# Kernel optimization log

Hardware: AMD Instinct MI355X
Metric: run time of the kernel (lower is better)

Reference implementation:

```python
import jax, jax.numpy as jnp
import numpy as np

B, T, E, H = 4, 2048, 1024, 16
HS = E // H  # head_size = 64


def setup_inputs() -> dict:
    key = jax.random.key(0)
    ks = jax.random.split(key, 5)
    x = jax.random.normal(ks[0], (B, T, E), jnp.float32)
    scale = 0.02
    Wq = jax.random.normal(ks[1], (H, E, HS), jnp.float32) * scale
    Wk = jax.random.normal(ks[2], (H, E, HS), jnp.float32) * scale
    Wv = jax.random.normal(ks[3], (H, E, HS), jnp.float32) * scale
    Wo = jax.random.normal(ks[4], (E, E), jnp.float32) * scale
    bo = jnp.zeros((E,), jnp.float32)
    return {"x": x, "Wq": Wq, "Wk": Wk, "Wv": Wv, "Wo": Wo, "bo": bo}


def reference(x, Wq, Wk, Wv, Wo, bo):
    b, t, e = x.shape
    # per-head projections, batched over heads
    Q = jnp.einsum('bte,hed->bhtd', x, Wq)  # (B,H,T,HS)
    K = jnp.einsum('bte,hed->bhtd', x, Wk)
    V = jnp.einsum('bte,hed->bhtd', x, Wv)
    # faithful quirk 1: scale by sqrt(embd_size), not sqrt(head_size)
    scores = jnp.einsum('bhtd,bhsd->bhts', Q, K) / jnp.sqrt(jnp.float32(e))
    mask = jnp.tril(jnp.ones((t, t), dtype=bool))  # (T_q, T_k)
    scores = jnp.where(mask[None, None, :, :], scores, -jnp.inf)
    # faithful quirk 2: original softmaxes over dim=1 of (B,Tq,Tk) = the QUERY axis
    attn = jax.nn.softmax(scores, axis=2)
    out = jnp.einsum('bhts,bhsd->bhtd', attn, V)  # (B,H,T,HS)
    out = out.transpose(0, 2, 1, 3).reshape(b, t, e)  # concat heads -> (B,T,E)
    return out @ Wo + bo
```

## Files before the change

kernel.cpp:

```cpp
#include <hip/hip_runtime.h>
#include <stdint.h>

#define Bn 4
#define Tn 2048
#define En 1024
#define Hn 16
#define HSn 64
#define BHn (Bn*Hn)
#define NRn (Bn*Tn)

#define CEXP 0.0450840831f

typedef __attribute__((ext_vector_type(8))) short short8;
typedef __attribute__((ext_vector_type(4))) float f32x4;
typedef __attribute__((ext_vector_type(16))) float f32x16;
typedef __attribute__((ext_vector_type(4))) unsigned int uint4w;

__device__ __forceinline__ unsigned short f2b(float f){
  union { float f; unsigned int u; } c; c.f = f;
  unsigned int u = c.u + 0x7FFFu + ((c.u >> 16) & 1u);
  return (unsigned short)(u >> 16);
}
__device__ __forceinline__ float b2f(unsigned short s){
  union { unsigned int u; float f; } c; c.u = ((unsigned int)s) << 16;
  return c.f;
}
__device__ __forceinline__ unsigned int cvtpk(float lo, float hi){
  unsigned int r;
  asm("v_cvt_pk_bf16_f32 %0, %1, %2" : "=v"(r) : "v"(lo), "v"(hi));
  return r;
}
__device__ __forceinline__ f32x4 mfma16(short8 a, short8 b, f32x4 c){
  return __builtin_amdgcn_mfma_f32_16x16x32_bf16(a, b, c, 0, 0, 0);
}
__device__ __forceinline__ f32x16 mfma32(short8 a, short8 b, f32x16 c){
  return __builtin_amdgcn_mfma_f32_32x32x16_bf16(a, b, c, 0, 0, 0);
}
__device__ __forceinline__ void gl16(const void* g, void* s){
  __builtin_amdgcn_global_load_lds((const __attribute__((address_space(1))) unsigned int*)g,
                                   (__attribute__((address_space(3))) unsigned int*)s, 16, 0, 0);
}
#define FENCE()    asm volatile("" ::: "memory")
#define WAITV(N)   asm volatile("s_waitcnt vmcnt(" #N ")" ::: "memory")
#define SBAR()     __builtin_amdgcn_s_barrier()

__global__ void k_cvt_x(const float* __restrict__ x, unsigned short* __restrict__ xb){
  int i = (blockIdx.x * blockDim.x + threadIdx.x) * 8;
  float4 a = *(const float4*)(x + i);
  float4 b = *(const float4*)(x + i + 4);
  alignas(16) unsigned short o[8] = {f2b(a.x),f2b(a.y),f2b(a.z),f2b(a.w),
                                     f2b(b.x),f2b(b.y),f2b(b.z),f2b(b.w)};
  *(uint4w*)(xb + i) = *(const uint4w*)o;
}

__global__ void k_wT(const float* __restrict__ Wq, const float* __restrict__ Wk,
                     const float* __restrict__ Wv, const float* __restrict__ Wo,
                     unsigned short* __restrict__ Wt, unsigned short* __restrict__ Wot)
{
  __shared__ unsigned short Ls[64*80];
  const int tid = threadIdx.x;
  const int ey = blockIdx.x, jt = blockIdx.y;
  const int e0 = ey*64;
  const float* src; int R, c0; unsigned short* outp;
  if (jt < 48){
    int sel = jt >> 4, h = jt & 15;
    const float* W = (sel==0)?Wq:((sel==1)?Wk:Wv);
    src = W + h*(En*HSn); R = HSn; c0 = 0;
    outp = Wt + jt*64*En;
  } else {
    src = Wo; R = En; c0 = (jt-48)*64;
    outp = Wot + (jt-48)*64*En;
  }
  {
    const int e = tid >> 2, cq = (tid & 3)*16;
    const float* p = src + (e0 + e)*R + c0 + cq;
    float vv[16];
    *(float4*)&vv[0]  = *(const float4*)(p);
    *(float4*)&vv[4]  = *(const float4*)(p+4);
    *(float4*)&vv[8]  = *(const float4*)(p+8);
    *(float4*)&vv[12] = *(const float4*)(p+12);
#pragma unroll
    for (int i = 0; i < 16; i++) Ls[(cq+i)*80 + e] = f2b(vv[i]);
  }
  __syncthreads();
  {
    const int c8 = tid & 7, r = tid >> 3;
#pragma unroll
    for (int rr0 = 0; rr0 < 2; rr0++){
      int rr = r + rr0*32;
      *(uint4w*)(outp + rr*En + e0 + c8*8) = *(const uint4w*)&Ls[rr*80 + c8*8];
    }
  }
}

__global__ void __launch_bounds__(256, 2)
k_qkv(const unsigned short* __restrict__ xb,
      const unsigned short* __restrict__ Wt,
      unsigned short* __restrict__ Qb, unsigned short* __restrict__ Kb,
      unsigned short* __restrict__ Vt)
{
  __shared__ unsigned short As[2][128*64];
  __shared__ unsigned short Bs[2][128*64];
  const int tid = threadIdx.x, lane = tid & 63, w = tid >> 6;
  const int wr = w >> 1, wc = w & 1;
  const int mb = blockIdx.x, nb = blockIdx.y;
  const int n0 = nb*128;
  const int sel = n0 >> 10;
  const int nj0 = n0 & 1023;
  const int l15 = lane & 15, kc = lane >> 4;
  const int r8 = lane >> 3, c7 = lane & 7;

  const unsigned short* xbase = xb + (mb*128)*En;
  const unsigned short* wbase = Wt + n0*En;

  f32x4 acc[4][4];
#pragma unroll
  for (int i = 0; i < 4; i++)
#pragma unroll
    for (int j = 0; j < 4; j++) acc[i][j] = (f32x4){0.f,0.f,0.f,0.f};

  auto stage = [&](int buf, int k0){
#pragma unroll
    for (int i = 0; i < 4; i++){
      const int rb = w*32 + i*8;
      const int r = rb + r8;
      const int g = (c7 ^ r8) * 8;
      gl16(xbase + r*En + k0 + g, &As[buf][rb*64]);
      gl16(wbase + r*En + k0 + g, &Bs[buf][rb*64]);
    }
  };
  auto compute = [&](int cur){
    const unsigned short* Ac = &As[cur][0];
    const unsigned short* Bc = &Bs[cur][0];
#pragma unroll
    for (int ks = 0; ks < 2; ks++){
      short8 af[4], bf[4];
#pragma unroll
      for (int mf = 0; mf < 4; mf++){
        int ar = wr*64 + mf*16 + l15;
        af[mf] = *(const short8*)&Ac[ar*64 + (((ks*4 + kc) ^ (ar & 7))*8)];
      }
#pragma unroll
      for (int nf = 0; nf < 4; nf++){
        int br = wc*64 + nf*16 + l15;
        bf[nf] = *(const short8*)&Bc[br*64 + (((ks*4 + kc) ^ (br & 7))*8)];
      }
      __builtin_amdgcn_s_setprio(1);
#pragma unroll
      for (int mf = 0; mf < 4; mf++)
#pragma unroll
        for (int nf = 0; nf < 4; nf++)
          acc[mf][nf] = mfma16(af[mf], bf[nf], acc[mf][nf]);
      __builtin_amdgcn_s_setprio(0);
    }
  };

  stage(0, 0);
  stage(1, 64);
  WAITV(8); SBAR();

  for (int kt = 0; kt < 16; kt++){
    const int cur = kt & 1;
    compute(cur);
    FENCE(); SBAR();
    if (kt < 14){
      stage(cur, (kt + 2)*64);
      WAITV(8); SBAR();
    } else if (kt == 14){
      WAITV(0); SBAR();
    }
  }
  __syncthreads();

  const int q4 = (lane >> 4)*4;
  const int bb = mb >> 4;
  const int tt0 = (mb*128) & 2047;

  if (sel == 2){
    unsigned short* tb = ((w < 2) ? &As[0][0] : &Bs[0][0]) + (w & 1)*8192;
#pragma unroll
    for (int nf = 0; nf < 4; nf++)
#pragma unroll
      for (int mf = 0; mf < 4; mf++){
        uint2 u;
        u.x = cvtpk(acc[mf][nf][0], acc[mf][nf][1]);
        u.y = cvtpk(acc[mf][nf][2], acc[mf][nf][3]);
        *(uint2*)&tb[(nf*16 + l15)*72 + mf*16 + q4] = u;
      }
    const int hh = (nj0 >> 6) + wc;
    unsigned short* vb = Vt + ((bb*Hn + hh)*HSn)*Tn + tt0 + wr*64;
#pragma unroll
    for (int i = 0; i < 8; i++){
      int rr = i*8 + r8;
      *(uint4w*)(vb + rr*Tn + c7*8) = *(const uint4w*)&tb[rr*72 + c7*8];
    }
  } else {
    unsigned short* Out = (sel == 1) ? Kb : Qb;
#pragma unroll
    for (int nf = 0; nf < 4; nf++){
      int jj = nj0 + wc*64 + nf*16 + l15;
      int hh = jj >> 6, dd = jj & 63;
#pragma unroll
      for (int mf = 0; mf < 4; mf++){
#pragma unroll
        for (int q = 0; q < 4; q++){
          int tt = tt0 + wr*64 + mf*16 + q4 + q;
          Out[((bb*Hn + hh)*Tn + tt)*HSn + dd] = f2b(acc[mf][nf][q]);
        }
      }
    }
  }
}

__global__ void __launch_bounds__(256, 3)
k_colsum(const unsigned short* __restrict__ Qb,
         const unsigned short* __restrict__ Kb,
         unsigned short* __restrict__ Vt,
         float* __restrict__ Linv)
{
  __shared__ unsigned short Qs[3][128*64];
  __shared__ float Lred[64];
  const int bh = blockIdx.x, ipair = blockIdx.y;
  const int tid = threadIdx.x, lane = tid & 63, w = tid >> 6;
  const int l5 = lane >> 5, l31 = lane & 31;
  const int r8 = lane >> 3, c7 = lane & 7;

  for (int ph = 0; ph < 2; ph++){
    const int sb = ph ? (31 - ipair) : ipair;
    const int s0 = sb * 64;

    short8 kf[2][4];
#pragma unroll
    for (int sf = 0; sf < 2; sf++){
      const unsigned short* kr = Kb + (bh*Tn + s0 + sf*32 + l31)*HSn + 8*l5;
#pragma unroll
      for (int ks = 0; ks < 4; ks++) kf[sf][ks] = *(const short8*)(kr + 16*ks);
    }

    float ls[2][16];
#pragma unroll
    for (int sf = 0; sf < 2; sf++)
#pragma unroll
      for (int r = 0; r < 16; r++) ls[sf][r] = 0.f;

    if (tid < 64) Lred[tid] = 0.f;

    const int t0s = (s0 >> 7) << 7;
    const int ntl = (Tn - t0s) >> 7;

    auto stageQ = [&](int buf, int tg0){
#pragma unroll
      for (int i = 0; i < 4; i++){
        int row = (w*4 + i)*8 + r8;
        gl16(Qb + (bh*Tn + tg0 + row)*HSn + ((c7 ^ (row & 7))*8), &Qs[buf][(w*4 + i)*512]);
      }
    };

    stageQ(0, t0s);
    if (ntl > 1) stageQ(1, t0s + 128);

    for (int it = 0; it < ntl; it++){
      if (it + 1 < ntl){ WAITV(4); } else { WAITV(0); }
      FENCE(); SBAR(); FENCE();
      if (it + 2 < ntl) stageQ((it + 2) % 3, t0s + (it + 2)*128);

      const int cur = it % 3;
      const int t0 = t0s + it*128;
      const int tw = t0 + 32*w;
      if (tw + 31 >= s0){
        f32x16 st[2];
#pragma unroll
        for (int sf = 0; sf < 2; sf++)
#pragma unroll
          for (int r = 0; r < 16; r++) st[sf][r] = 0.f;
        const int qrow = w*32 + l31;
        const unsigned short* Qc = &Qs[cur][qrow*64];
        const int sw = qrow & 7;
        __builtin_amdgcn_s_setprio(1);
#pragma unroll
        for (int ks = 0; ks < 4; ks++){
          short8 qb = *(const short8*)&Qc[((l5 + 2*ks) ^ sw)*8];
          st[0] = mfma32(kf[0][ks], qb, st[0]);
          st[1] = mfma32(kf[1][ks], qb, st[1]);
        }
        __builtin_amdgcn_s_setprio(0);
        const int tg = tw + l31;
        if (s0 + 63 <= tw){
#pragma unroll
          for (int sf = 0; sf < 2; sf++)
#pragma unroll
            for (int r = 0; r < 16; r++)
              ls[sf][r] += __builtin_amdgcn_exp2f(st[sf][r] * CEXP);
        } else {
#pragma unroll
          for (int sf = 0; sf < 2; sf++)
#pragma unroll
            for (int r = 0; r < 16; r++){
              int sg = s0 + 32*sf + (r & 3) + 8*(r >> 2) + 4*l5;
              float e = __builtin_amdgcn_exp2f(st[sf][r] * CEXP);
              ls[sf][r] += (tg >= sg) ? e : 0.f;
            }
        }
      }
    }

#pragma unroll
    for (int sf = 0; sf < 2; sf++)
#pragma unroll
      for (int r = 0; r < 16; r++){
        float v = ls[sf][r];
        v += __shfl_xor(v, 1);  v += __shfl_xor(v, 2);
        v += __shfl_xor(v, 4);  v += __shfl_xor(v, 8);
        v += __shfl_xor(v, 16);
        ls[sf][r] = v;
      }
    if (l31 == 0){
#pragma unroll
      for (int sf = 0; sf < 2; sf++)
#pragma unroll
        for (int r = 0; r < 16; r++){
          int sl = 32*sf + (r & 3) + 8*(r >> 2) + 4*l5;
          atomicAdd(&Lred[sl], ls[sf][r]);
        }
    }
    __syncthreads();
    if (tid < 64) Linv[bh*Tn + s0 + tid] = 1.0f / Lred[tid];

    {
      const int d = tid >> 2, cq = (tid & 3)*16;
      unsigned short* vp = Vt + ((size_t)(bh*HSn + d))*Tn + s0 + cq;
      short8 v0 = *(const short8*)vp;
      short8 v1 = *(const short8*)(vp + 8);
      float inv[16];
#pragma unroll
      for (int j = 0; j < 16; j++) inv[j] = 1.0f / Lred[cq + j];
      uint4w o0, o1;
      o0[0] = cvtpk(b2f((unsigned short)v0[0])*inv[0],  b2f((unsigned short)v0[1])*inv[1]);
      o0[1] = cvtpk(b2f((unsigned short)v0[2])*inv[2],  b2f((unsigned short)v0[3])*inv[3]);
      o0[2] = cvtpk(b2f((unsigned short)v0[4])*inv[4],  b2f((unsigned short)v0[5])*inv[5]);
      o0[3] = cvtpk(b2f((unsigned short)v0[6])*inv[6],  b2f((unsigned short)v0[7])*inv[7]);
      o1[0] = cvtpk(b2f((unsigned short)v1[0])*inv[8],  b2f((unsigned short)v1[1])*inv[9]);
      o1[1] = cvtpk(b2f((unsigned short)v1[2])*inv[10], b2f((unsigned short)v1[3])*inv[11]);
      o1[2] = cvtpk(b2f((unsigned short)v1[4])*inv[12], b2f((unsigned short)v1[5])*inv[13]);
      o1[3] = cvtpk(b2f((unsigned short)v1[6])*inv[14], b2f((unsigned short)v1[7])*inv[15]);
      *(uint4w*)vp       = o0;
      *(uint4w*)(vp + 8) = o1;
    }
    if (ph == 0) __syncthreads();
  }
}

__global__ void __launch_bounds__(256, 3)
k_attn(const unsigned short* __restrict__ Qb,
       const unsigned short* __restrict__ Kb,
       const unsigned short* __restrict__ Vlt,
       unsigned short* __restrict__ Att)
{
  __shared__ unsigned short Ks[3][64*64];
  __shared__ unsigned short Vs[3][64*64];
  const int bh = blockIdx.x;
  const int tb = 15 - blockIdx.y;
  const int t0 = tb * 128;
  const int tid = threadIdx.x, lane = tid & 63, w = tid >> 6;
  const int l5 = lane >> 5, l31 = lane & 31;
  const int c7 = lane & 7, r8 = lane >> 3;
  const int tbase = t0 + w*32;
  const int nt = 2*tb + 2;

  short8 qf[4];
  {
    const unsigned short* qr = Qb + (bh*Tn + tbase + l31)*HSn + 8*l5;
#pragma unroll
    for (int ks = 0; ks < 4; ks++) qf[ks] = *(const short8*)(qr + 16*ks);
  }

  f32x16 oacc[2];
#pragma unroll
  for (int df = 0; df < 2; df++)
#pragma unroll
    for (int r = 0; r < 16; r++) oacc[df][r] = 0.f;

  auto stageKV = [&](int buf, int sn){
#pragma unroll
    for (int i = 0; i < 2; i++){
      int row = (w*2 + i)*8 + r8;
      gl16(Kb  + (bh*Tn + sn + row)*HSn + ((c7 ^ (row & 7))*8), &Ks[buf][(w*2 + i)*512]);
      gl16(Vlt + (bh*HSn + row)*Tn + sn + ((c7 ^ (row & 7))*8), &Vs[buf][(w*2 + i)*512]);
    }
  };

  stageKV(0, 0);
  if (nt > 1) stageKV(1, 64);

  for (int it = 0; it < nt; it++){
    if (it + 1 < nt){ WAITV(4); } else { WAITV(0); }
    FENCE(); SBAR(); FENCE();
    if (it + 2 < nt) stageKV((it + 2) % 3, (it + 2)*64);

    const int cur = it % 3;
    const int s0 = it * 64;
    if (s0 <= tbase + 31){
      const unsigned short* Kc = &Ks[cur][0];
      f32x16 st[2];
#pragma unroll
      for (int sf = 0; sf < 2; sf++)
#pragma unroll
        for (int r = 0; r < 16; r++) st[sf][r] = 0.f;
      __builtin_amdgcn_s_setprio(1);
#pragma unroll
      for (int ks = 0; ks < 4; ks++){
#pragma unroll
        for (int sf = 0; sf < 2; sf++){
          int row = sf*32 + l31;
          short8 ka = *(const short8*)&Kc[row*64 + (((l5 + 2*ks) ^ (row & 7))*8)];
          st[sf] = mfma32(ka, qf[ks], st[sf]);
        }
      }
      __builtin_amdgcn_s_setprio(0);

      const int tg = tbase + l31;
      const bool interior = (s0 + 63 <= tbase);
#pragma unroll
      for (int sf = 0; sf < 2; sf++){
#pragma unroll
        for (int r = 0; r < 16; r++){
          float e = __builtin_amdgcn_exp2f(st[sf][r] * CEXP);
          if (!interior){
            int sg = s0 + 32*sf + (r & 3) + 8*(r >> 2) + 4*l5;
            e = (tg >= sg) ? e : 0.f;
          }
          st[sf][r] = e;
        }
      }

      short8 pb[4];
#pragma unroll
      for (int sf = 0; sf < 2; sf++){
#pragma unroll
        for (int q = 0; q < 2; q++){
          unsigned int ax = cvtpk(st[sf][8*q+0], st[sf][8*q+1]);
          unsigned int ay = cvtpk(st[sf][8*q+2], st[sf][8*q+3]);
          unsigned int bx = cvtpk(st[sf][8*q+4], st[sf][8*q+5]);
          unsigned int by = cvtpk(st[sf][8*q+6], st[sf][8*q+7]);
          asm("v_permlane32_swap_b32 %0, %1" : "+v"(ax), "+v"(bx));
          asm("v_permlane32_swap_b32 %0, %1" : "+v"(ay), "+v"(by));
          union { unsigned int u[4]; short8 s; } pk;
          pk.u[0] = ax; pk.u[1] = ay; pk.u[2] = bx; pk.u[3] = by;
          pb[sf*2 + q] = pk.s;
        }
      }

      const unsigned short* Vc = &Vs[cur][0];
      __builtin_amdgcn_s_setprio(1);
#pragma unroll
      for (int ks = 0; ks < 4; ks++){
#pragma unroll
        for (int df = 0; df < 2; df++){
          int row = df*32 + l31;
          short8 va = *(const short8*)&Vc[row*64 + (((l5 + 2*ks) ^ (row & 7))*8)];
          oacc[df] = mfma32(va, pb[ks], oacc[df]);
        }
      }
      __builtin_amdgcn_s_setprio(0);
    }
  }

  {
    const int tg = tbase + l31;
    unsigned short* ob = Att + (bh*Tn + tg)*HSn;
#pragma unroll
    for (int df = 0; df < 2; df++)
#pragma unroll
      for (int r2 = 0; r2 < 4; r2++){
        uint2 u;
        u.x = cvtpk(oacc[df][r2*4+0], oacc[df][r2*4+1]);
        u.y = cvtpk(oacc[df][r2*4+2], oacc[df][r2*4+3]);
        *(uint2*)&ob[32*df + 8*r2 + 4*l5] = u;
      }
  }
}

__global__ void __launch_bounds__(256, 2)
k_oproj(const unsigned short* __restrict__ Att,
        const unsigned short* __restrict__ Wot,
        const float* __restrict__ bo, float* __restrict__ out)
{
  __shared__ unsigned short As[2][128*64];
  __shared__ unsigned short Bs[2][128*64];
  const int tid = threadIdx.x, lane = tid & 63, w = tid >> 6;
  const int wr = w >> 1, wc = w & 1;
  const int mb = blockIdx.x, nb = blockIdx.y;
  const int n0 = nb*128;
  const int l15 = lane & 15, kc = lane >> 4;
  const int r8 = lane >> 3, c7 = lane & 7;
  const int bb = mb >> 4;
  const int t0 = (mb*128) & 2047;

  f32x4 acc[4][4];
#pragma unroll
  for (int i = 0; i < 4; i++)
#pragma unroll
    for (int j = 0; j < 4; j++) acc[i][j] = (f32x4){0.f,0.f,0.f,0.f};

  const unsigned short* wbase = Wot + n0*En;

  auto stage = [&](int buf, int k0){
    const int hh = k0 >> 6;
    const unsigned short* abase = Att + ((bb*Hn + hh)*Tn + t0)*HSn;
#pragma unroll
    for (int i = 0; i < 4; i++){
      const int rb = w*32 + i*8;
      const int r = rb + r8;
      const int g = (c7 ^ r8) * 8;
      gl16(abase + r*HSn + g, &As[buf][rb*64]);
      gl16(wbase + r*En + k0 + g, &Bs[buf][rb*64]);
    }
  };
  auto compute = [&](int cur){
    const unsigned short* Ac = &As[cur][0];
    const unsigned short* Bc = &Bs[cur][0];
#pragma unroll
    for (int ks = 0; ks < 2; ks++){
      short8 af[4], bf[4];
#pragma unroll
      for (int mf = 0; mf < 4; mf++){
        int ar = wr*64 + mf*16 + l15;
        af[mf] = *(const short8*)&Ac[ar*64 + (((ks*4 + kc) ^ (ar & 7))*8)];
      }
#pragma unroll
      for (int nf = 0; nf < 4; nf++){
        int br = wc*64 + nf*16 + l15;
        bf[nf] = *(const short8*)&Bc[br*64 + (((ks*4 + kc) ^ (br & 7))*8)];
      }
      __builtin_amdgcn_s_setprio(1);
#pragma unroll
      for (int mf = 0; mf < 4; mf++)
#pragma unroll
        for (int nf = 0; nf < 4; nf++)
          acc[mf][nf] = mfma16(af[mf], bf[nf], acc[mf][nf]);
      __builtin_amdgcn_s_setprio(0);
    }
  };

  stage(0, 0);
  stage(1, 64);
  WAITV(8); SBAR();

  for (int kt = 0; kt < 16; kt++){
    const int cur = kt & 1;
    compute(cur);
    FENCE(); SBAR();
    if (kt < 14){
      stage(cur, (kt + 2)*64);
      WAITV(8); SBAR();
    } else if (kt == 14){
      WAITV(0); SBAR();
    }
  }

  const int q4 = (lane >> 4)*4;
#pragma unroll
  for (int nf = 0; nf < 4; nf++){
    int j = n0 + wc*64 + nf*16 + l15;
    float bias = bo[j];
#pragma unroll
    for (int mf = 0; mf < 4; mf++){
#pragma unroll
      for (int q = 0; q < 4; q++){
        int rr = mb*128 + wr*64 + mf*16 + q4 + q;
        out[rr*En + j] = acc[mf][nf][q] + bias;
      }
    }
  }
}

extern "C" void kernel_launch(void* const* d_in, const int* in_sizes, int n_in,
                              void* d_out, int out_size, void* d_ws, size_t ws_size,
                              hipStream_t stream)
{
  (void)in_sizes; (void)n_in; (void)out_size; (void)ws_size;
  const float* x  = (const float*)d_in[0];
  const float* Wq = (const float*)d_in[1];
  const float* Wk = (const float*)d_in[2];
  const float* Wv = (const float*)d_in[3];
  const float* Wo = (const float*)d_in[4];
  const float* bo = (const float*)d_in[5];
  float* out = (float*)d_out;

  uint8_t* w = (uint8_t*)d_ws;
  unsigned short* Qb  = (unsigned short*)(w);
  unsigned short* Kb  = (unsigned short*)(w + (16u << 20));
  unsigned short* Vt  = (unsigned short*)(w + (32u << 20));
  unsigned short* xb  = (unsigned short*)(w + (48u << 20));
  unsigned short* Att = (unsigned short*)(w + (48u << 20));
  unsigned short* Wt  = (unsigned short*)(w + (64u << 20));
  unsigned short* Wot = (unsigned short*)(w + (70u << 20));
  float* Linv         = (float*)(w + (72u << 20));

  hipLaunchKernelGGL(k_cvt_x,  dim3(4096),    dim3(256), 0, stream, x, xb);
  hipLaunchKernelGGL(k_wT,     dim3(16, 64),  dim3(256), 0, stream, Wq, Wk, Wv, Wo, Wt, Wot);
  hipLaunchKernelGGL(k_qkv,    dim3(64, 24),  dim3(256), 0, stream, xb, Wt, Qb, Kb, Vt);
  hipLaunchKernelGGL(k_colsum, dim3(64, 16),  dim3(256), 0, stream, Qb, Kb, Vt, Linv);
  hipLaunchKernelGGL(k_attn,   dim3(64, 16),  dim3(256), 0, stream, Qb, Kb, Vt, Att);
  hipLaunchKernelGGL(k_oproj,  dim3(64, 8),   dim3(256), 0, stream, Att, Wot, bo, out);
}
```

Measured before the change: 208.0 us.

## Fold softmax scale into Wq, split colsum blocks, remap grids for locality

The exp2 scale constant is folded into Wq during the weight conversion, so the colsum and attention kernels skip a multiply per score. The colsum kernel no longer pairs two column blocks per workgroup via a loop; it launches one block per key tile (8x256 grid) and iterates query tiles in reverse order. Both colsum and attn remap block indices so that 8 consecutive heads share a blockIdx.x slice, changing scheduling order and cache locality. Folding the scale into Q before bf16 rounding slightly alters numerics, and the unpaired colsum grid loses the load balancing that pairing gave.

```diff
diff --git a/kernel.cpp b/kernel.cpp
--- a/kernel.cpp
+++ b/kernel.cpp
@@ -61,10 +61,11 @@
   const int tid = threadIdx.x;
   const int ey = blockIdx.x, jt = blockIdx.y;
   const int e0 = ey*64;
-  const float* src; int R, c0; unsigned short* outp;
+  const float* src; int R, c0; unsigned short* outp; float sc = 1.0f;
   if (jt < 48){
     int sel = jt >> 4, h = jt & 15;
     const float* W = (sel==0)?Wq:((sel==1)?Wk:Wv);
+    if (sel == 0) sc = CEXP;
     src = W + h*(En*HSn); R = HSn; c0 = 0;
     outp = Wt + jt*64*En;
   } else {
@@ -80,7 +81,7 @@
     *(float4*)&vv[8]  = *(const float4*)(p+8);
     *(float4*)&vv[12] = *(const float4*)(p+12);
 #pragma unroll
-    for (int i = 0; i < 16; i++) Ls[(cq+i)*80 + e] = f2b(vv[i]);
+    for (int i = 0; i < 16; i++) Ls[(cq+i)*80 + e] = f2b(vv[i]*sc);
   }
   __syncthreads();
   {
@@ -220,133 +221,129 @@
 {
   __shared__ unsigned short Qs[3][128*64];
   __shared__ float Lred[64];
-  const int bh = blockIdx.x, ipair = blockIdx.y;
+  const int bh = blockIdx.x*8 + (blockIdx.y & 7);
+  const int sb = blockIdx.y >> 3;
+  const int s0 = sb * 64;
   const int tid = threadIdx.x, lane = tid & 63, w = tid >> 6;
   const int l5 = lane >> 5, l31 = lane & 31;
   const int r8 = lane >> 3, c7 = lane & 7;
 
-  for (int ph = 0; ph < 2; ph++){
-    const int sb = ph ? (31 - ipair) : ipair;
-    const int s0 = sb * 64;
-
-    short8 kf[2][4];
-#pragma unroll
-    for (int sf = 0; sf < 2; sf++){
-      const unsigned short* kr = Kb + (bh*Tn + s0 + sf*32 + l31)*HSn + 8*l5;
-#pragma unroll
-      for (int ks = 0; ks < 4; ks++) kf[sf][ks] = *(const short8*)(kr + 16*ks);
-    }
-
-    float ls[2][16];
+  short8 kf[2][4];
+#pragma unroll
+  for (int sf = 0; sf < 2; sf++){
+    const unsigned short* kr = Kb + (bh*Tn + s0 + sf*32 + l31)*HSn + 8*l5;
+#pragma unroll
+    for (int ks = 0; ks < 4; ks++) kf[sf][ks] = *(const short8*)(kr + 16*ks);
+  }
+
+  float ls[2][16];
+#pragma unroll
+  for (int sf = 0; sf < 2; sf++)
+#pragma unroll
+    for (int r = 0; r < 16; r++) ls[sf][r] = 0.f;
+
+  if (tid < 64) Lred[tid] = 0.f;
+
+  const int t0s = (s0 >> 7) << 7;
+  const int ntl = (Tn - t0s) >> 7;
+
+  auto stageQ = [&](int buf, int tg0){
+#pragma unroll
+    for (int i = 0; i < 4; i++){
+      int row = (w*4 + i)*8 + r8;
+      gl16(Qb + (bh*Tn + tg0 + row)*HSn + ((c7 ^ (row & 7))*8), &Qs[buf][(w*4 + i)*512]);
+    }
+  };
+
+  stageQ(0, t0s + (ntl-1)*128);
+  if (ntl > 1) stageQ(1, t0s + (ntl-2)*128);
+
+  for (int j = 0; j < ntl; j++){
+    if (j + 1 < ntl){ WAITV(4); } else { WAITV(0); }
+    FENCE(); SBAR(); FENCE();
+    if (j + 2 < ntl) stageQ((j + 2) % 3, t0s + (ntl-3-j)*128);
+
+    const int cur = j % 3;
+    const int t0 = t0s + (ntl-1-j)*128;
+    const int tw = t0 + 32*w;
+    if (tw + 31 >= s0){
+      f32x16 st[2];
+#pragma unroll
+      for (int sf = 0; sf < 2; sf++)
+#pragma unroll
+        for (int r = 0; r < 16; r++) st[sf][r] = 0.f;
+      const int qrow = w*32 + l31;
+      const unsigned short* Qc = &Qs[cur][qrow*64];
+      const int sw = qrow & 7;
+      __builtin_amdgcn_s_setprio(1);
+#pragma unroll
+      for (int ks = 0; ks < 4; ks++){
+        short8 qb = *(const short8*)&Qc[((l5 + 2*ks) ^ sw)*8];
+        st[0] = mfma32(kf[0][ks], qb, st[0]);
+        st[1] = mfma32(kf[1][ks], qb, st[1]);
+      }
+      __builtin_amdgcn_s_setprio(0);
+      const int tg = tw + l31;
+      if (s0 + 63 <= tw){
+#pragma unroll
+        for (int sf = 0; sf < 2; sf++)
+#pragma unroll
+          for (int r = 0; r < 16; r++)
+            ls[sf][r] += __builtin_amdgcn_exp2f(st[sf][r]);
+      } else {
+#pragma unroll
+        for (int sf = 0; sf < 2; sf++)
+#pragma unroll
+          for (int r = 0; r < 16; r++){
+            int sg = s0 + 32*sf + (r & 3) + 8*(r >> 2) + 4*l5;
+            float e = __builtin_amdgcn_exp2f(st[sf][r]);
+            ls[sf][r] += (tg >= sg) ? e : 0.f;
+          }
+      }
+    }
+  }
+
+#pragma unroll
+  for (int sf = 0; sf < 2; sf++)
+#pragma unroll
+    for (int r = 0; r < 16; r++){
+      float v = ls[sf][r];
+      v += __shfl_xor(v, 1);  v += __shfl_xor(v, 2);
+      v += __shfl_xor(v, 4);  v += __shfl_xor(v, 8);
+      v += __shfl_xor(v, 16);
+      ls[sf][r] = v;
+    }
+  if (l31 == 0){
 #pragma unroll
     for (int sf = 0; sf < 2; sf++)
 #pragma unroll
-      for (int r = 0; r < 16; r++) ls[sf][r] = 0.f;
-
-    if (tid < 64) Lred[tid] = 0.f;
-
-    const int t0s = (s0 >> 7) << 7;
-    const int ntl = (Tn - t0s) >> 7;
-
-    auto stageQ = [&](int buf, int tg0){
-#pragma unroll
-      for (int i = 0; i < 4; i++){
-        int row = (w*4 + i)*8 + r8;
-        gl16(Qb + (bh*Tn + tg0 + row)*HSn + ((c7 ^ (row & 7))*8), &Qs[buf][(w*4 + i)*512]);
-      }
-    };
-
-    stageQ(0, t0s);
-    if (ntl > 1) stageQ(1, t0s + 128);
-
-    for (int it = 0; it < ntl; it++){
-      if (it + 1 < ntl){ WAITV(4); } else { WAITV(0); }
-      FENCE(); SBAR(); FENCE();
-      if (it + 2 < ntl) stageQ((it + 2) % 3, t0s + (it + 2)*128);
-
-      const int cur = it % 3;
-      const int t0 = t0s + it*128;
-      const int tw = t0 + 32*w;
-      if (tw + 31 >= s0){
-        f32x16 st[2];
-#pragma unroll
-        for (int sf = 0; sf < 2; sf++)
-#pragma unroll
-          for (int r = 0; r < 16; r++) st[sf][r] = 0.f;
-        const int qrow = w*32 + l31;
-        const unsigned short* Qc = &Qs[cur][qrow*64];
-        const int sw = qrow & 7;
-        __builtin_amdgcn_s_setprio(1);
-#pragma unroll
-        for (int ks = 0; ks < 4; ks++){
-          short8 qb = *(const short8*)&Qc[((l5 + 2*ks) ^ sw)*8];
-          st[0] = mfma32(kf[0][ks], qb, st[0]);
-          st[1] = mfma32(kf[1][ks], qb, st[1]);
-        }
-        __builtin_amdgcn_s_setprio(0);
-        const int tg = tw + l31;
-        if (s0 + 63 <= tw){
-#pragma unroll
-          for (int sf = 0; sf < 2; sf++)
-#pragma unroll
-            for (int r = 0; r < 16; r++)
-              ls[sf][r] += __builtin_amdgcn_exp2f(st[sf][r] * CEXP);
-        } else {
-#pragma unroll
-          for (int sf = 0; sf < 2; sf++)
-#pragma unroll
-            for (int r = 0; r < 16; r++){
-              int sg = s0 + 32*sf + (r & 3) + 8*(r >> 2) + 4*l5;
-              float e = __builtin_amdgcn_exp2f(st[sf][r] * CEXP);
-              ls[sf][r] += (tg >= sg) ? e : 0.f;
-            }
-        }
-      }
-    }
-
-#pragma unroll
-    for (int sf = 0; sf < 2; sf++)
-#pragma unroll
       for (int r = 0; r < 16; r++){
-        float v = ls[sf][r];
-        v += __shfl_xor(v, 1);  v += __shfl_xor(v, 2);
-        v += __shfl_xor(v, 4);  v += __shfl_xor(v, 8);
-        v += __shfl_xor(v, 16);
-        ls[sf][r] = v;
-      }
-    if (l31 == 0){
-#pragma unroll
-      for (int sf = 0; sf < 2; sf++)
-#pragma unroll
-        for (int r = 0; r < 16; r++){
-          int sl = 32*sf + (r & 3) + 8*(r >> 2) + 4*l5;
-          atomicAdd(&Lred[sl], ls[sf][r]);
-        }
-    }
-    __syncthreads();
-    if (tid < 64) Linv[bh*Tn + s0 + tid] = 1.0f / Lred[tid];
-
-    {
-      const int d = tid >> 2, cq = (tid & 3)*16;
-      unsigned short* vp = Vt + ((size_t)(bh*HSn + d))*Tn + s0 + cq;
-      short8 v0 = *(const short8*)vp;
-      short8 v1 = *(const short8*)(vp + 8);
-      float inv[16];
-#pragma unroll
-      for (int j = 0; j < 16; j++) inv[j] = 1.0f / Lred[cq + j];
-      uint4w o0, o1;
-      o0[0] = cvtpk(b2f((unsigned short)v0[0])*inv[0],  b2f((unsigned short)v0[1])*inv[1]);
-      o0[1] = cvtpk(b2f((unsigned short)v0[2])*inv[2],  b2f((unsigned short)v0[3])*inv[3]);
-      o0[2] = cvtpk(b2f((unsigned short)v0[4])*inv[4],  b2f((unsigned short)v0[5])*inv[5]);
-      o0[3] = cvtpk(b2f((unsigned short)v0[6])*inv[6],  b2f((unsigned short)v0[7])*inv[7]);
-      o1[0] = cvtpk(b2f((unsigned short)v1[0])*inv[8],  b2f((unsigned short)v1[1])*inv[9]);
-      o1[1] = cvtpk(b2f((unsigned short)v1[2])*inv[10], b2f((unsigned short)v1[3])*inv[11]);
-      o1[2] = cvtpk(b2f((unsigned short)v1[4])*inv[12], b2f((unsigned short)v1[5])*inv[13]);
-      o1[3] = cvtpk(b2f((unsigned short)v1[6])*inv[14], b2f((unsigned short)v1[7])*inv[15]);
-      *(uint4w*)vp       = o0;
-      *(uint4w*)(vp + 8) = o1;
-    }
-    if (ph == 0) __syncthreads();
+        int sl = 32*sf + (r & 3) + 8*(r >> 2) + 4*l5;
+        atomicAdd(&Lred[sl], ls[sf][r]);
+      }
+  }
+  __syncthreads();
+  if (tid < 64) Linv[bh*Tn + s0 + tid] = 1.0f / Lred[tid];
+
+  {
+    const int d = tid >> 2, cq = (tid & 3)*16;
+    unsigned short* vp = Vt + ((size_t)(bh*HSn + d))*Tn + s0 + cq;
+    short8 v0 = *(const short8*)vp;
+    short8 v1 = *(const short8*)(vp + 8);
+    float inv[16];
+#pragma unroll
+    for (int j = 0; j < 16; j++) inv[j] = 1.0f / Lred[cq + j];
+    uint4w o0, o1;
+    o0[0] = cvtpk(b2f((unsigned short)v0[0])*inv[0],  b2f((unsigned short)v0[1])*inv[1]);
+    o0[1] = cvtpk(b2f((unsigned short)v0[2])*inv[2],  b2f((unsigned short)v0[3])*inv[3]);
+    o0[2] = cvtpk(b2f((unsigned short)v0[4])*inv[4],  b2f((unsigned short)v0[5])*inv[5]);
+    o0[3] = cvtpk(b2f((unsigned short)v0[6])*inv[6],  b2f((unsigned short)v0[7])*inv[7]);
+    o1[0] = cvtpk(b2f((unsigned short)v1[0])*inv[8],  b2f((unsigned short)v1[1])*inv[9]);
+    o1[1] = cvtpk(b2f((unsigned short)v1[2])*inv[10], b2f((unsigned short)v1[3])*inv[11]);
+    o1[2] = cvtpk(b2f((unsigned short)v1[4])*inv[12], b2f((unsigned short)v1[5])*inv[13]);
+    o1[3] = cvtpk(b2f((unsigned short)v1[6])*inv[14], b2f((unsigned short)v1[7])*inv[15]);
+    *(uint4w*)vp       = o0;
+    *(uint4w*)(vp + 8) = o1;
   }
 }
 
@@ -358,8 +355,8 @@
 {
   __shared__ unsigned short Ks[3][64*64];
   __shared__ unsigned short Vs[3][64*64];
-  const int bh = blockIdx.x;
-  const int tb = 15 - blockIdx.y;
+  const int bh = blockIdx.x*8 + (blockIdx.y & 7);
+  const int tb = 15 - (blockIdx.y >> 3);
   const int t0 = tb * 128;
   const int tid = threadIdx.x, lane = tid & 63, w = tid >> 6;
   const int l5 = lane >> 5, l31 = lane & 31;
@@ -424,7 +421,7 @@
       for (int sf = 0; sf < 2; sf++){
 #pragma unroll
         for (int r = 0; r < 16; r++){
-          float e = __builtin_amdgcn_exp2f(st[sf][r] * CEXP);
+          float e = __builtin_amdgcn_exp2f(st[sf][r]);
           if (!interior){
             int sg = s0 + 32*sf + (r & 3) + 8*(r >> 2) + 4*l5;
             e = (tg >= sg) ? e : 0.f;
@@ -600,7 +597,7 @@
   hipLaunchKernelGGL(k_cvt_x,  dim3(4096),    dim3(256), 0, stream, x, xb);
   hipLaunchKernelGGL(k_wT,     dim3(16, 64),  dim3(256), 0, stream, Wq, Wk, Wv, Wo, Wt, Wot);
   hipLaunchKernelGGL(k_qkv,    dim3(64, 24),  dim3(256), 0, stream, xb, Wt, Qb, Kb, Vt);
-  hipLaunchKernelGGL(k_colsum, dim3(64, 16),  dim3(256), 0, stream, Qb, Kb, Vt, Linv);
-  hipLaunchKernelGGL(k_attn,   dim3(64, 16),  dim3(256), 0, stream, Qb, Kb, Vt, Att);
+  hipLaunchKernelGGL(k_colsum, dim3(8, 256),  dim3(256), 0, stream, Qb, Kb, Vt, Linv);
+  hipLaunchKernelGGL(k_attn,   dim3(8, 128),  dim3(256), 0, stream, Qb, Kb, Vt, Att);
   hipLaunchKernelGGL(k_oproj,  dim3(64, 8),   dim3(256), 0, stream, Att, Wot, bo, out);
 }
```

Measured after the change: 199.2 us. 1.04x faster.
